# Optimization experiments

Measured on AMD Instinct MI355X. Metric: run time of the kernel, lower is better.

## Reference

```python
import jax, jax.numpy as jnp
import numpy as np

N_HEADS = 16
HEAD_DIM = 64


def apply_rope(x, cos, sin):
    # x: [B, H, S, D]; cos/sin: [S, D//2]
    x_even = x[..., ::2]
    x_odd = x[..., 1::2]
    c = cos[None, None, :, :]
    s = sin[None, None, :, :]
    rot_even = x_even * c - x_odd * s
    rot_odd = x_even * s + x_odd * c
    return jnp.stack((rot_even, rot_odd), axis=-1).reshape(x.shape)


def setup_inputs() -> dict:
    key = jax.random.key(0)
    ks = jax.random.split(key, 7)
    B, S, D = 2, 2048, 1024
    x = jax.random.normal(ks[0], (B, S, D), dtype=jnp.float32)
    # realistic rope tables
    inv_freq = 1.0 / (10000.0 ** (np.arange(0, HEAD_DIM, 2, dtype=np.float32) / HEAD_DIM))
    t = np.arange(S, dtype=np.float32)
    freqs = np.outer(t, inv_freq)  # [S, HEAD_DIM//2]
    rope_cos = jnp.asarray(np.cos(freqs), dtype=jnp.float32)
    rope_sin = jnp.asarray(np.sin(freqs), dtype=jnp.float32)
    Wqkv = jax.random.normal(ks[1], (D, 3 * D), dtype=jnp.float32) * (D ** -0.5)
    bqkv = jax.random.normal(ks[2], (3 * D,), dtype=jnp.float32) * 0.02
    Wout = jax.random.normal(ks[3], (D, D), dtype=jnp.float32) * (D ** -0.5)
    bout = jax.random.normal(ks[4], (D,), dtype=jnp.float32) * 0.02
    return {"x": x, "rope_cos": rope_cos, "rope_sin": rope_sin,
            "Wqkv": Wqkv, "bqkv": bqkv, "Wout": Wout, "bout": bout}


def reference(x, rope_cos, rope_sin, Wqkv, bqkv, Wout, bout):
    B, S, D = x.shape
    H, Hd = N_HEADS, HEAD_DIM
    qkv = x @ Wqkv + bqkv                      # [B, S, 3D]
    qkv = qkv.reshape(B, S, 3, H, Hd).transpose(2, 0, 3, 1, 4)  # [3, B, H, S, Hd]
    q, k, v = qkv[0], qkv[1], qkv[2]
    q = apply_rope(q, rope_cos, rope_sin)
    k = apply_rope(k, rope_cos, rope_sin)
    scale = Hd ** -0.5
    scores = jnp.einsum('bhqd,bhkd->bhqk', q, k) * scale
    causal = jnp.tril(jnp.ones((S, S), dtype=bool))
    scores = jnp.where(causal[None, None], scores, jnp.finfo(scores.dtype).min)
    attn = jax.nn.softmax(scores, axis=-1)
    out = jnp.einsum('bhqk,bhkd->bhqd', attn, v)  # [B, H, S, Hd]
    out = out.transpose(0, 2, 1, 3).reshape(B, S, D)
    return out @ Wout + bout
```

## Files before the change

### kernel.cpp

```cpp
#include <hip/hip_runtime.h>
#include <hip/hip_bf16.h>

typedef unsigned short u16;
typedef __attribute__((ext_vector_type(4))) float f32x4;
typedef __attribute__((ext_vector_type(16))) float f32x16;
typedef __attribute__((ext_vector_type(8))) short short8;
typedef __attribute__((ext_vector_type(8))) unsigned short ushort8;

#define AS1 __attribute__((address_space(1)))
#define AS3 __attribute__((address_space(3)))

__device__ __forceinline__ u16 f2bf(float f) {
  union { float f; unsigned u; } v; v.f = f;
  unsigned r = v.u + 0x7fffu + ((v.u >> 16) & 1u);
  return (u16)(r >> 16);
}
__device__ __forceinline__ float b2f(u16 h) {
  union { unsigned u; float f; } v; v.u = ((unsigned)h) << 16;
  return v.f;
}
__device__ __forceinline__ f32x4 mfma16(short8 a, short8 b, f32x4 c) {
  return __builtin_amdgcn_mfma_f32_16x16x32_bf16(a, b, c, 0, 0, 0);
}
__device__ __forceinline__ f32x16 mfma32(short8 a, short8 b, f32x16 c) {
  return __builtin_amdgcn_mfma_f32_32x32x16_bf16(a, b, c, 0, 0, 0);
}
__device__ __forceinline__ unsigned cvtpk(float a, float b) {
  unsigned r;
  asm("v_cvt_pk_bf16_f32 %0, %1, %2" : "=v"(r) : "v"(a), "v"(b));
  return r;
}
__device__ __forceinline__ short8 pack4(unsigned w0, unsigned w1, unsigned w2, unsigned w3) {
  union { unsigned u[4]; short8 s; } t;
  t.u[0] = w0; t.u[1] = w1; t.u[2] = w2; t.u[3] = w3;
  return t.s;
}
__device__ __forceinline__ float exp2h(float x) { return __builtin_amdgcn_exp2f(x); }

__global__ __launch_bounds__(256) void cvt_f32_bf16_k(const float* __restrict__ in,
                                                      u16* __restrict__ out, int n8) {
  int t = blockIdx.x * 256 + threadIdx.x;
  if (t >= n8) return;
  const float4* p = (const float4*)(in + (size_t)t * 8);
  float4 a = p[0], b = p[1];
  ushort8 o;
  o[0] = f2bf(a.x); o[1] = f2bf(a.y); o[2] = f2bf(a.z); o[3] = f2bf(a.w);
  o[4] = f2bf(b.x); o[5] = f2bf(b.y); o[6] = f2bf(b.z); o[7] = f2bf(b.w);
  *(ushort8*)(out + (size_t)t * 8) = o;
}

__global__ __launch_bounds__(256) void transpose_f32_bf16_k(const float* __restrict__ in,
                                                            u16* __restrict__ out, int R, int C) {
  __shared__ float tile[32][33];
  int bc = blockIdx.x * 32, br = blockIdx.y * 32;
  int tx = threadIdx.x & 31, ty = threadIdx.x >> 5;
#pragma unroll
  for (int p = 0; p < 4; ++p)
    tile[ty + p * 8][tx] = in[(size_t)(br + ty + p * 8) * C + bc + tx];
  __syncthreads();
#pragma unroll
  for (int p = 0; p < 4; ++p)
    out[(size_t)(bc + ty + p * 8) * R + br + tx] = f2bf(tile[tx][ty + p * 8]);
}

template <int MODE>
__global__ __launch_bounds__(256) void gemm_bt_k(const u16* __restrict__ A,
                                                 const u16* __restrict__ Bt,
                                                 const float* __restrict__ bias,
                                                 const float* __restrict__ cosT,
                                                 const float* __restrict__ sinT,
                                                 void* __restrict__ Cout) {
  __shared__ __align__(16) u16 As[128 * 32];
  __shared__ __align__(16) u16 Bs[128 * 32];
  const int tid = threadIdx.x, lane = tid & 63, w = tid >> 6;
  const int wr = w >> 1, wc = w & 1, g = lane >> 4, c16 = lane & 15;
  const int rowBase = blockIdx.y * 128, colBase = blockIdx.x * 128;
  f32x4 acc[4][4] = {};
  const int e0 = (w * 2 + 0) * 512 + lane * 8;
  const int e1 = (w * 2 + 1) * 512 + lane * 8;
  const u16* Ag0 = A + (size_t)(rowBase + (e0 >> 5)) * 1024 + (e0 & 31);
  const u16* Ag1 = A + (size_t)(rowBase + (e1 >> 5)) * 1024 + (e1 & 31);
  const u16* Bg0 = Bt + (size_t)(colBase + (e0 >> 5)) * 1024 + (e0 & 31);
  const u16* Bg1 = Bt + (size_t)(colBase + (e1 >> 5)) * 1024 + (e1 & 31);
  u16* As0 = As + (w * 2 + 0) * 512;
  u16* As1 = As + (w * 2 + 1) * 512;
  u16* Bs0 = Bs + (w * 2 + 0) * 512;
  u16* Bs1 = Bs + (w * 2 + 1) * 512;
  for (int k0 = 0; k0 < 1024; k0 += 32) {
    __builtin_amdgcn_global_load_lds((const AS1 void*)(Ag0 + k0), (AS3 void*)As0, 16, 0, 0);
    __builtin_amdgcn_global_load_lds((const AS1 void*)(Ag1 + k0), (AS3 void*)As1, 16, 0, 0);
    __builtin_amdgcn_global_load_lds((const AS1 void*)(Bg0 + k0), (AS3 void*)Bs0, 16, 0, 0);
    __builtin_amdgcn_global_load_lds((const AS1 void*)(Bg1 + k0), (AS3 void*)Bs1, 16, 0, 0);
    asm volatile("s_waitcnt vmcnt(0)" ::: "memory");
    __syncthreads();
    short8 af[4], bfr[4];
#pragma unroll
    for (int t = 0; t < 4; ++t)
      af[t] = *(const short8*)(As + ((wr * 64 + t * 16 + c16) * 32 + g * 8));
#pragma unroll
    for (int t = 0; t < 4; ++t)
      bfr[t] = *(const short8*)(Bs + ((wc * 64 + t * 16 + c16) * 32 + g * 8));
#pragma unroll
    for (int i = 0; i < 4; ++i)
#pragma unroll
      for (int j = 0; j < 4; ++j) acc[i][j] = mfma16(af[i], bfr[j], acc[i][j]);
    __syncthreads();
  }
#pragma unroll
  for (int i = 0; i < 4; ++i) {
    int mbase = rowBase + wr * 64 + i * 16 + 4 * g;
#pragma unroll
    for (int j = 0; j < 4; ++j) {
      int n = colBase + wc * 64 + j * 16 + c16;
      float bv = bias[n];
#pragma unroll
      for (int r = 0; r < 4; ++r) {
        float v = acc[i][j][r] + bv;
        int m = mbase + r;
        if (MODE == 0) {
          int which = n >> 10, hh = (n >> 6) & 15, d = n & 63;
          int bb = m >> 11, s = m & 2047;
          float outv = v;
          if (which < 2) {
            float pv = __shfl_xor(v, 1);
            float cc = cosT[(size_t)s * 32 + (d >> 1)];
            float ss = sinT[(size_t)s * 32 + (d >> 1)];
            outv = (d & 1) ? (v * cc + pv * ss) : (v * cc - pv * ss);
            if (which == 0) outv *= 0.18033688f;
          }
          ((u16*)Cout)[((size_t)(((which * 2 + bb) * 16 + hh) * 2048 + s) << 6) + d] = f2bf(outv);
        } else {
          ((float*)Cout)[(size_t)m * 1024 + n] = v;
        }
      }
    }
  }
}

__global__ __launch_bounds__(256) void vtrans_k(const u16* __restrict__ V, u16* __restrict__ Vt) {
  __shared__ u16 t[64][72];
  const int bh = blockIdx.y, s0 = blockIdx.x * 64;
  const u16* src = V + ((size_t)bh << 17);
  u16* dst = Vt + ((size_t)bh << 17);
  const int r = threadIdx.x >> 2, c0 = (threadIdx.x & 3) * 16;
  *(short8*)&t[r][c0] = *(const short8*)(src + (size_t)(s0 + r) * 64 + c0);
  *(short8*)&t[r][c0 + 8] = *(const short8*)(src + (size_t)(s0 + r) * 64 + c0 + 8);
  __syncthreads();
  const int d = threadIdx.x >> 2, sc0 = (threadIdx.x & 3) * 16;
  ushort8 o0, o1;
#pragma unroll
  for (int e = 0; e < 8; ++e) { o0[e] = t[sc0 + e][d]; o1[e] = t[sc0 + 8 + e][d]; }
  *(ushort8*)(dst + (size_t)d * 2048 + s0 + sc0) = o0;
  *(ushort8*)(dst + (size_t)d * 2048 + s0 + sc0 + 8) = o1;
}

__global__ __launch_bounds__(128, 4) void attn8_k(const u16* __restrict__ Qm,
                                                  const u16* __restrict__ Km,
                                                  const u16* __restrict__ Vtm,
                                                  u16* __restrict__ Om) {
  __shared__ __align__(16) u16 KL[2][4096];
  __shared__ __align__(16) u16 VL[2][4096];

  const int tid = threadIdx.x;
  const int lane = tid & 63, w = tid >> 6;
  const int x = blockIdx.x & 7;
  const int i = blockIdx.x >> 3;
  const int bh = 4 * x + (i & 3);
  const int rank = i >> 2;
  const int sl = rank >> 3, g8 = rank & 7;
  const int qm = (sl & 1) ? (8 * sl + 7 - g8) : (8 * sl + g8);
  const int b = bh >> 4, hd = bh & 15;
  const int qb = qm * 64 + w * 32;
  const int q32 = lane & 31, hl = lane >> 5;
  const int nt = qm + 1;

  const u16* Qp = Qm + ((size_t)bh << 17);
  const u16* Kp = Km + ((size_t)bh << 17);
  const u16* Vtp = Vtm + ((size_t)bh << 17);

  const u16* qrow = Qp + ((size_t)(qb + q32) << 6) + 8 * hl;
  short8 qf[4];
#pragma unroll
  for (int ks = 0; ks < 4; ++ks) qf[ks] = *(const short8*)(qrow + 16 * ks);

  f32x16 acc0 = {}, acc1 = {};
  float m_run = -1e30f, l_run = 0.f;
  const int qg = qb + q32;
  const int r8 = lane >> 3;
  const int sb = (lane & 7) ^ r8;
  const int swz = q32 & 7;

  auto stage = [&](int buf, int k0s) {
#pragma unroll
    for (int j = 0; j < 4; ++j) {
      const int row = j * 16 + w * 8 + r8;
      const u16* ksrc = Kp + ((size_t)(k0s + row) << 6) + sb * 8;
      __builtin_amdgcn_global_load_lds(
          (const AS1 void*)ksrc,
          (AS3 void*)(&KL[buf][(j * 16 + w * 8) * 64]), 16, 0, 0);
      const u16* vsrc = Vtp + ((size_t)row << 11) + k0s + sb * 8;
      __builtin_amdgcn_global_load_lds(
          (const AS1 void*)vsrc,
          (AS3 void*)(&VL[buf][(j * 16 + w * 8) * 64]), 16, 0, 0);
    }
  };

  stage(0, 0);
  asm volatile("s_waitcnt vmcnt(0)" ::: "memory");
  __syncthreads();

  for (int it = 0; it < nt; ++it) {
    const int cur = it & 1;
    if (it + 1 < nt) stage(cur ^ 1, 64 * (it + 1));
    const int k0 = 64 * it;

    const u16* Kb = &KL[cur][0];
    const u16* Vb = &VL[cur][0];

    f32x16 s0 = {}, s1 = {};
    __builtin_amdgcn_s_setprio(1);
#pragma unroll
    for (int ks = 0; ks < 4; ++ks) {
      const int cb = ((2 * ks + hl) ^ swz) * 8;
      short8 kf0 = *(const short8*)(Kb + q32 * 64 + cb);
      short8 kf1 = *(const short8*)(Kb + (32 + q32) * 64 + cb);
      s0 = mfma32(kf0, qf[ks], s0);
      s1 = mfma32(kf1, qf[ks], s1);
    }
    __builtin_amdgcn_s_setprio(0);

    short8 vfa[4], vfb[4];
#pragma unroll
    for (int ks = 0; ks < 4; ++ks) {
      const int cb = ((2 * ks + hl) ^ swz) * 8;
      vfa[ks] = *(const short8*)(Vb + q32 * 64 + cb);
      vfb[ks] = *(const short8*)(Vb + (32 + q32) * 64 + cb);
    }

    if (k0 + 63 > qb) {
#pragma unroll
      for (int r = 0; r < 16; ++r) {
        const int kvl = k0 + (r & 3) + 8 * (r >> 2) + 4 * hl;
        s0[r] = (kvl <= qg) ? s0[r] : -1e30f;
        s1[r] = (kvl + 32 <= qg) ? s1[r] : -1e30f;
      }
    }

    float pmax = s0[0];
#pragma unroll
    for (int r = 1; r < 16; ++r) pmax = fmaxf(pmax, s0[r]);
#pragma unroll
    for (int r = 0; r < 16; ++r) pmax = fmaxf(pmax, s1[r]);
    pmax = fmaxf(pmax, __shfl_xor(pmax, 32));

    if (!__all(pmax <= m_run + 11.5f)) {
      const float mn = fmaxf(m_run, pmax);
      const float alpha = exp2h(m_run - mn);
      l_run *= alpha;
      m_run = mn;
#pragma unroll
      for (int r = 0; r < 16; ++r) {
        const int row = (r & 3) + 8 * (r >> 2) + 4 * hl;
        const float ar = __shfl(alpha, row);
        acc0[r] *= ar; acc1[r] *= ar;
      }
    }

    float rs = 0.f;
#pragma unroll
    for (int r = 0; r < 16; ++r) { s0[r] = exp2h(s0[r] - m_run); rs += s0[r]; }
#pragma unroll
    for (int r = 0; r < 16; ++r) { s1[r] = exp2h(s1[r] - m_run); rs += s1[r]; }
    rs += __shfl_xor(rs, 32);
    l_run += rs;

    short8 pa[4];
#pragma unroll
    for (int t = 0; t < 2; ++t) {
      float p0, p1, p2, p3, p4, p5, p6, p7, p8, p9, pa_, pb_, pc_, pd_, pe_, pf_;
      if (t == 0) {
        p0 = s0[0];  p1 = s0[1];  p2 = s0[2];  p3 = s0[3];
        p4 = s0[4];  p5 = s0[5];  p6 = s0[6];  p7 = s0[7];
        p8 = s0[8];  p9 = s0[9];  pa_ = s0[10]; pb_ = s0[11];
        pc_ = s0[12]; pd_ = s0[13]; pe_ = s0[14]; pf_ = s0[15];
      } else {
        p0 = s1[0];  p1 = s1[1];  p2 = s1[2];  p3 = s1[3];
        p4 = s1[4];  p5 = s1[5];  p6 = s1[6];  p7 = s1[7];
        p8 = s1[8];  p9 = s1[9];  pa_ = s1[10]; pb_ = s1[11];
        pc_ = s1[12]; pd_ = s1[13]; pe_ = s1[14]; pf_ = s1[15];
      }
      const unsigned a0 = cvtpk(p0, p1), a1 = cvtpk(p2, p3);
      const unsigned a2 = cvtpk(p4, p5), a3 = cvtpk(p6, p7);
      const unsigned b0 = cvtpk(p8, p9), b1 = cvtpk(pa_, pb_);
      const unsigned b2 = cvtpk(pc_, pd_), b3 = cvtpk(pe_, pf_);
      const unsigned r0 = __shfl_xor(hl ? a0 : a2, 32);
      const unsigned r1 = __shfl_xor(hl ? a1 : a3, 32);
      pa[2 * t] = hl ? pack4(r0, r1, a2, a3) : pack4(a0, a1, r0, r1);
      const unsigned r2 = __shfl_xor(hl ? b0 : b2, 32);
      const unsigned r3 = __shfl_xor(hl ? b1 : b3, 32);
      pa[2 * t + 1] = hl ? pack4(r2, r3, b2, b3) : pack4(b0, b1, r2, r3);
    }

    __builtin_amdgcn_s_setprio(1);
#pragma unroll
    for (int ks = 0; ks < 4; ++ks) {
      acc0 = mfma32(pa[ks], vfa[ks], acc0);
      acc1 = mfma32(pa[ks], vfb[ks], acc1);
    }
    __builtin_amdgcn_s_setprio(0);

    asm volatile("s_waitcnt vmcnt(0)" ::: "memory");
    __syncthreads();
  }

#pragma unroll
  for (int r = 0; r < 16; ++r) {
    const int row = (r & 3) + 8 * (r >> 2) + 4 * hl;
    const float li = 1.0f / __shfl(l_run, row);
    const int q = qb + row;
    const size_t base = ((size_t)(b * 2048 + q) << 10) + hd * 64 + q32;
    Om[base] = f2bf(acc0[r] * li);
    Om[base + 32] = f2bf(acc1[r] * li);
  }
}

extern "C" void kernel_launch(void* const* d_in, const int* in_sizes, int n_in,
                              void* d_out, int out_size, void* d_ws, size_t ws_size,
                              hipStream_t stream) {
  const float* x        = (const float*)d_in[0];
  const float* rope_cos = (const float*)d_in[1];
  const float* rope_sin = (const float*)d_in[2];
  const float* Wqkv     = (const float*)d_in[3];
  const float* bqkv     = (const float*)d_in[4];
  const float* Wout     = (const float*)d_in[5];
  const float* bout     = (const float*)d_in[6];
  float* out = (float*)d_out;
  char* ws = (char*)d_ws;

  u16* Xb      = (u16*)(ws);
  u16* WqkvT   = (u16*)(ws + 8388608);
  u16* WoutT   = (u16*)(ws + 14680064);
  u16* QKV     = (u16*)(ws + 16777216);
  u16* AttnOut = (u16*)(ws + 41943040);
  u16* Vt      = (u16*)(ws + 50331648);

  cvt_f32_bf16_k<<<dim3(2048), dim3(256), 0, stream>>>(x, Xb, 524288);
  transpose_f32_bf16_k<<<dim3(96, 32), dim3(256), 0, stream>>>(Wqkv, WqkvT, 1024, 3072);
  transpose_f32_bf16_k<<<dim3(32, 32), dim3(256), 0, stream>>>(Wout, WoutT, 1024, 1024);

  gemm_bt_k<0><<<dim3(24, 32), dim3(256), 0, stream>>>(Xb, WqkvT, bqkv, rope_cos, rope_sin,
                                                       (void*)QKV);

  u16* Qw = QKV;
  u16* Kw = QKV + (size_t)4194304;
  u16* Vw = QKV + (size_t)8388608;
  vtrans_k<<<dim3(32, 32), dim3(256), 0, stream>>>(Vw, Vt);
  attn8_k<<<dim3(1024), dim3(128), 0, stream>>>(Qw, Kw, Vt, AttnOut);

  gemm_bt_k<1><<<dim3(8, 32), dim3(256), 0, stream>>>(AttnOut, WoutT, bout, nullptr, nullptr, out);
}
```

Measured before the change: 145.0 us.

## Enlarge attention tiles to 128 queries and 128 keys per block with four waves

The attention kernel now uses 256-thread blocks that each own 128 query rows, and it processes 128-key tiles per iteration with double-buffered K and V in LDS. The V tile gets a new swizzle. V fragments are loaded just in time inside each PV sub-step, and sub-tiles lying entirely above the diagonal are skipped on the last tile. The aim is to halve the grid and the number of loop iterations, sharing each staged K/V tile across more query rows to cut global traffic and sync overhead. In exchange it uses more LDS and registers per block, lowers occupancy, and increases load imbalance from the causal structure, since the block order changes from 1024 to 512 blocks.

```diff
diff --git a/kernel.cpp b/kernel.cpp
--- a/kernel.cpp
+++ b/kernel.cpp
@@ -154,12 +154,12 @@
   *(ushort8*)(dst + (size_t)d * 2048 + s0 + sc0 + 8) = o1;
 }
 
-__global__ __launch_bounds__(128, 4) void attn8_k(const u16* __restrict__ Qm,
+__global__ __launch_bounds__(256, 2) void attn9_k(const u16* __restrict__ Qm,
                                                   const u16* __restrict__ Km,
                                                   const u16* __restrict__ Vtm,
                                                   u16* __restrict__ Om) {
-  __shared__ __align__(16) u16 KL[2][4096];
-  __shared__ __align__(16) u16 VL[2][4096];
+  __shared__ __align__(16) u16 KL[2][8192];
+  __shared__ __align__(16) u16 VL[2][8192];
 
   const int tid = threadIdx.x;
   const int lane = tid & 63, w = tid >> 6;
@@ -167,10 +167,9 @@
   const int i = blockIdx.x >> 3;
   const int bh = 4 * x + (i & 3);
   const int rank = i >> 2;
-  const int sl = rank >> 3, g8 = rank & 7;
-  const int qm = (sl & 1) ? (8 * sl + 7 - g8) : (8 * sl + g8);
+  const int qm = (rank < 8) ? (15 - rank) : (rank - 8);
   const int b = bh >> 4, hd = bh & 15;
-  const int qb = qm * 64 + w * 32;
+  const int qb = qm * 128 + w * 32;
   const int q32 = lane & 31, hl = lane >> 5;
   const int nt = qm + 1;
 
@@ -185,23 +184,25 @@
 
   f32x16 acc0 = {}, acc1 = {};
   float m_run = -1e30f, l_run = 0.f;
-  const int qg = qb + q32;
-  const int r8 = lane >> 3;
-  const int sb = (lane & 7) ^ r8;
   const int swz = q32 & 7;
+  const int swz4 = q32 & 15;
+  const int kr = lane >> 3;
+  const int kcb = (lane & 7) ^ kr;
+  const int vr = lane >> 4;
 
   auto stage = [&](int buf, int k0s) {
 #pragma unroll
     for (int j = 0; j < 4; ++j) {
-      const int row = j * 16 + w * 8 + r8;
-      const u16* ksrc = Kp + ((size_t)(k0s + row) << 6) + sb * 8;
+      const int ck = w * 4 + j;
+      const int krow = ck * 8 + kr;
       __builtin_amdgcn_global_load_lds(
-          (const AS1 void*)ksrc,
-          (AS3 void*)(&KL[buf][(j * 16 + w * 8) * 64]), 16, 0, 0);
-      const u16* vsrc = Vtp + ((size_t)row << 11) + k0s + sb * 8;
+          (const AS1 void*)(Kp + ((size_t)(k0s + krow) << 6) + kcb * 8),
+          (AS3 void*)(&KL[buf][ck * 512]), 16, 0, 0);
+      const int vrow = ck * 4 + vr;
+      const int vcb = (lane & 15) ^ (vrow & 15);
       __builtin_amdgcn_global_load_lds(
-          (const AS1 void*)vsrc,
-          (AS3 void*)(&VL[buf][(j * 16 + w * 8) * 64]), 16, 0, 0);
+          (const AS1 void*)(Vtp + ((size_t)vrow << 11) + k0s + vcb * 8),
+          (AS3 void*)(&VL[buf][ck * 512]), 16, 0, 0);
     }
   };
 
@@ -209,40 +210,35 @@
   asm volatile("s_waitcnt vmcnt(0)" ::: "memory");
   __syncthreads();
 
-  for (int it = 0; it < nt; ++it) {
-    const int cur = it & 1;
-    if (it + 1 < nt) stage(cur ^ 1, 64 * (it + 1));
-    const int k0 = 64 * it;
+  for (int kt = 0; kt < nt; ++kt) {
+    const int cur = kt & 1;
+    if (kt + 1 < nt) stage(cur ^ 1, 128 * (kt + 1));
+    const bool last = (kt == nt - 1);
 
     const u16* Kb = &KL[cur][0];
     const u16* Vb = &VL[cur][0];
 
-    f32x16 s0 = {}, s1 = {};
+    f32x16 s0 = {}, s1 = {}, s2 = {}, s3 = {};
     __builtin_amdgcn_s_setprio(1);
 #pragma unroll
     for (int ks = 0; ks < 4; ++ks) {
       const int cb = ((2 * ks + hl) ^ swz) * 8;
-      short8 kf0 = *(const short8*)(Kb + q32 * 64 + cb);
-      short8 kf1 = *(const short8*)(Kb + (32 + q32) * 64 + cb);
-      s0 = mfma32(kf0, qf[ks], s0);
-      s1 = mfma32(kf1, qf[ks], s1);
+      s0 = mfma32(*(const short8*)(Kb + (q32) * 64 + cb), qf[ks], s0);
+      s1 = mfma32(*(const short8*)(Kb + (32 + q32) * 64 + cb), qf[ks], s1);
+      s2 = mfma32(*(const short8*)(Kb + (64 + q32) * 64 + cb), qf[ks], s2);
+      s3 = mfma32(*(const short8*)(Kb + (96 + q32) * 64 + cb), qf[ks], s3);
     }
     __builtin_amdgcn_s_setprio(0);
 
-    short8 vfa[4], vfb[4];
-#pragma unroll
-    for (int ks = 0; ks < 4; ++ks) {
-      const int cb = ((2 * ks + hl) ^ swz) * 8;
-      vfa[ks] = *(const short8*)(Vb + q32 * 64 + cb);
-      vfb[ks] = *(const short8*)(Vb + (32 + q32) * 64 + cb);
-    }
-
-    if (k0 + 63 > qb) {
+    if (last) {
+      const int qloc = 32 * w + q32;
 #pragma unroll
       for (int r = 0; r < 16; ++r) {
-        const int kvl = k0 + (r & 3) + 8 * (r >> 2) + 4 * hl;
-        s0[r] = (kvl <= qg) ? s0[r] : -1e30f;
-        s1[r] = (kvl + 32 <= qg) ? s1[r] : -1e30f;
+        const int crow = (r & 3) + 8 * (r >> 2) + 4 * hl;
+        s0[r] = (crow <= qloc) ? s0[r] : -1e30f;
+        s1[r] = (32 + crow <= qloc) ? s1[r] : -1e30f;
+        s2[r] = (64 + crow <= qloc) ? s2[r] : -1e30f;
+        s3[r] = (96 + crow <= qloc) ? s3[r] : -1e30f;
       }
     }
 
@@ -251,6 +247,10 @@
     for (int r = 1; r < 16; ++r) pmax = fmaxf(pmax, s0[r]);
 #pragma unroll
     for (int r = 0; r < 16; ++r) pmax = fmaxf(pmax, s1[r]);
+#pragma unroll
+    for (int r = 0; r < 16; ++r) pmax = fmaxf(pmax, s2[r]);
+#pragma unroll
+    for (int r = 0; r < 16; ++r) pmax = fmaxf(pmax, s3[r]);
     pmax = fmaxf(pmax, __shfl_xor(pmax, 32));
 
     if (!__all(pmax <= m_run + 11.5f)) {
@@ -271,43 +271,44 @@
     for (int r = 0; r < 16; ++r) { s0[r] = exp2h(s0[r] - m_run); rs += s0[r]; }
 #pragma unroll
     for (int r = 0; r < 16; ++r) { s1[r] = exp2h(s1[r] - m_run); rs += s1[r]; }
+#pragma unroll
+    for (int r = 0; r < 16; ++r) { s2[r] = exp2h(s2[r] - m_run); rs += s2[r]; }
+#pragma unroll
+    for (int r = 0; r < 16; ++r) { s3[r] = exp2h(s3[r] - m_run); rs += s3[r]; }
     rs += __shfl_xor(rs, 32);
     l_run += rs;
 
-    short8 pa[4];
-#pragma unroll
-    for (int t = 0; t < 2; ++t) {
-      float p0, p1, p2, p3, p4, p5, p6, p7, p8, p9, pa_, pb_, pc_, pd_, pe_, pf_;
-      if (t == 0) {
-        p0 = s0[0];  p1 = s0[1];  p2 = s0[2];  p3 = s0[3];
-        p4 = s0[4];  p5 = s0[5];  p6 = s0[6];  p7 = s0[7];
-        p8 = s0[8];  p9 = s0[9];  pa_ = s0[10]; pb_ = s0[11];
-        pc_ = s0[12]; pd_ = s0[13]; pe_ = s0[14]; pf_ = s0[15];
-      } else {
-        p0 = s1[0];  p1 = s1[1];  p2 = s1[2];  p3 = s1[3];
-        p4 = s1[4];  p5 = s1[5];  p6 = s1[6];  p7 = s1[7];
-        p8 = s1[8];  p9 = s1[9];  pa_ = s1[10]; pb_ = s1[11];
-        pc_ = s1[12]; pd_ = s1[13]; pe_ = s1[14]; pf_ = s1[15];
-      }
-      const unsigned a0 = cvtpk(p0, p1), a1 = cvtpk(p2, p3);
-      const unsigned a2 = cvtpk(p4, p5), a3 = cvtpk(p6, p7);
-      const unsigned b0 = cvtpk(p8, p9), b1 = cvtpk(pa_, pb_);
-      const unsigned b2 = cvtpk(pc_, pd_), b3 = cvtpk(pe_, pf_);
-      const unsigned r0 = __shfl_xor(hl ? a0 : a2, 32);
-      const unsigned r1 = __shfl_xor(hl ? a1 : a3, 32);
-      pa[2 * t] = hl ? pack4(r0, r1, a2, a3) : pack4(a0, a1, r0, r1);
-      const unsigned r2 = __shfl_xor(hl ? b0 : b2, 32);
-      const unsigned r3 = __shfl_xor(hl ? b1 : b3, 32);
-      pa[2 * t + 1] = hl ? pack4(r2, r3, b2, b3) : pack4(b0, b1, r2, r3);
-    }
-
-    __builtin_amdgcn_s_setprio(1);
-#pragma unroll
-    for (int ks = 0; ks < 4; ++ks) {
-      acc0 = mfma32(pa[ks], vfa[ks], acc0);
-      acc1 = mfma32(pa[ks], vfb[ks], acc1);
-    }
-    __builtin_amdgcn_s_setprio(0);
+    auto pvsub = [&](const f32x16& sv, int t) {
+      short8 p0, p1;
+      {
+        const unsigned a0 = cvtpk(sv[0], sv[1]), a1 = cvtpk(sv[2], sv[3]);
+        const unsigned a2 = cvtpk(sv[4], sv[5]), a3 = cvtpk(sv[6], sv[7]);
+        const unsigned b0 = cvtpk(sv[8], sv[9]), b1 = cvtpk(sv[10], sv[11]);
+        const unsigned b2 = cvtpk(sv[12], sv[13]), b3 = cvtpk(sv[14], sv[15]);
+        const unsigned r0 = __shfl_xor(hl ? a0 : a2, 32);
+        const unsigned r1 = __shfl_xor(hl ? a1 : a3, 32);
+        p0 = hl ? pack4(r0, r1, a2, a3) : pack4(a0, a1, r0, r1);
+        const unsigned r2 = __shfl_xor(hl ? b0 : b2, 32);
+        const unsigned r3 = __shfl_xor(hl ? b1 : b3, 32);
+        p1 = hl ? pack4(r2, r3, b2, b3) : pack4(b0, b1, r2, r3);
+      }
+      __builtin_amdgcn_s_setprio(1);
+#pragma unroll
+      for (int j = 0; j < 2; ++j) {
+        const short8 pj = j ? p1 : p0;
+        const int cbv = ((4 * t + 2 * j + hl) ^ swz4) * 8;
+        const short8 vf0 = *(const short8*)(Vb + q32 * 128 + cbv);
+        const short8 vf1 = *(const short8*)(Vb + (32 + q32) * 128 + cbv);
+        acc0 = mfma32(pj, vf0, acc0);
+        acc1 = mfma32(pj, vf1, acc1);
+      }
+      __builtin_amdgcn_s_setprio(0);
+    };
+
+    pvsub(s0, 0);
+    if (!last || w >= 1) pvsub(s1, 1);
+    if (!last || w >= 2) pvsub(s2, 2);
+    if (!last || w >= 3) pvsub(s3, 3);
 
     asm volatile("s_waitcnt vmcnt(0)" ::: "memory");
     __syncthreads();
@@ -355,7 +356,7 @@
   u16* Kw = QKV + (size_t)4194304;
   u16* Vw = QKV + (size_t)8388608;
   vtrans_k<<<dim3(32, 32), dim3(256), 0, stream>>>(Vw, Vt);
-  attn8_k<<<dim3(1024), dim3(128), 0, stream>>>(Qw, Kw, Vt, AttnOut);
+  attn9_k<<<dim3(512), dim3(256), 0, stream>>>(Qw, Kw, Vt, AttnOut);
 
   gemm_bt_k<1><<<dim3(8, 32), dim3(256), 0, stream>>>(AttnOut, WoutT, bout, nullptr, nullptr, out);
 }
```

New measurement: 133.8 us. 1.08x faster.

## Use 128-row query blocks with split-KV for long rows plus merge kernel

Applied to the files above, without the earlier changes.

The attention kernel now uses 4 waves per block covering 128 query rows, so each staged K/V tile is shared by twice as many queries. For the upper 8 query blocks the KV range is split in two halves handled by separate blocks, each writing unnormalized bf16 partial accumulators and running max/sum to workspace. A new merge kernel combines the two halves. This is meant to cut K/V reload traffic and balance causal work across blocks, at the cost of an extra launch, partial-result traffic, bf16 rounding of the partials, and reuse of the Xb workspace region.

```diff
diff --git a/kernel.cpp b/kernel.cpp
--- a/kernel.cpp
+++ b/kernel.cpp
@@ -154,25 +154,28 @@
   *(ushort8*)(dst + (size_t)d * 2048 + s0 + sc0 + 8) = o1;
 }
 
-__global__ __launch_bounds__(128, 4) void attn8_k(const u16* __restrict__ Qm,
-                                                  const u16* __restrict__ Km,
-                                                  const u16* __restrict__ Vtm,
-                                                  u16* __restrict__ Om) {
+__global__ __launch_bounds__(256, 3) void attn10_k(const u16* __restrict__ Qm,
+                                                   const u16* __restrict__ Km,
+                                                   const u16* __restrict__ Vtm,
+                                                   u16* __restrict__ Pacc,
+                                                   float* __restrict__ Ml,
+                                                   u16* __restrict__ Om) {
   __shared__ __align__(16) u16 KL[2][4096];
   __shared__ __align__(16) u16 VL[2][4096];
 
   const int tid = threadIdx.x;
   const int lane = tid & 63, w = tid >> 6;
   const int x = blockIdx.x & 7;
-  const int i = blockIdx.x >> 3;
-  const int bh = 4 * x + (i & 3);
-  const int rank = i >> 2;
-  const int sl = rank >> 3, g8 = rank & 7;
-  const int qm = (sl & 1) ? (8 * sl + 7 - g8) : (8 * sl + g8);
+  const int idx = blockIdx.x >> 3;
+  const int j = idx & 3, u = idx >> 2;
+  const int bh = 4 * x + j;
+  int qm, t0, t1, half;
+  bool split;
+  if (u < 8) { qm = u; split = false; half = 0; t0 = 0; t1 = 2 * u + 2; }
+  else { split = true; half = (u >= 16); qm = 15 - (u & 7); t0 = half ? (qm + 1) : 0; t1 = t0 + qm + 1; }
   const int b = bh >> 4, hd = bh & 15;
-  const int qb = qm * 64 + w * 32;
+  const int qb = qm * 128 + w * 32;
   const int q32 = lane & 31, hl = lane >> 5;
-  const int nt = qm + 1;
 
   const u16* Qp = Qm + ((size_t)bh << 17);
   const u16* Kp = Km + ((size_t)bh << 17);
@@ -186,141 +189,193 @@
   f32x16 acc0 = {}, acc1 = {};
   float m_run = -1e30f, l_run = 0.f;
   const int qg = qb + q32;
-  const int r8 = lane >> 3;
-  const int sb = (lane & 7) ^ r8;
+  const int rr = w * 8 + (lane >> 3);
+  const int sb = (lane & 7) ^ (lane >> 3);
   const int swz = q32 & 7;
 
   auto stage = [&](int buf, int k0s) {
-#pragma unroll
-    for (int j = 0; j < 4; ++j) {
-      const int row = j * 16 + w * 8 + r8;
-      const u16* ksrc = Kp + ((size_t)(k0s + row) << 6) + sb * 8;
-      __builtin_amdgcn_global_load_lds(
-          (const AS1 void*)ksrc,
-          (AS3 void*)(&KL[buf][(j * 16 + w * 8) * 64]), 16, 0, 0);
-      const u16* vsrc = Vtp + ((size_t)row << 11) + k0s + sb * 8;
-      __builtin_amdgcn_global_load_lds(
-          (const AS1 void*)vsrc,
-          (AS3 void*)(&VL[buf][(j * 16 + w * 8) * 64]), 16, 0, 0);
-    }
+    u16* kb = &KL[buf][w * 512];
+    u16* vb = &VL[buf][w * 512];
+    __builtin_amdgcn_global_load_lds(
+        (const AS1 void*)(Kp + ((size_t)(k0s + rr) << 6) + sb * 8),
+        (AS3 void*)kb, 16, 0, 0);
+    __builtin_amdgcn_global_load_lds(
+        (const AS1 void*)(Kp + ((size_t)(k0s + rr + 32) << 6) + sb * 8),
+        (AS3 void*)(kb + 2048), 16, 0, 0);
+    __builtin_amdgcn_global_load_lds(
+        (const AS1 void*)(Vtp + ((size_t)rr << 11) + k0s + sb * 8),
+        (AS3 void*)vb, 16, 0, 0);
+    __builtin_amdgcn_global_load_lds(
+        (const AS1 void*)(Vtp + ((size_t)(rr + 32) << 11) + k0s + sb * 8),
+        (AS3 void*)(vb + 2048), 16, 0, 0);
   };
 
-  stage(0, 0);
+  stage(0, 64 * t0);
   asm volatile("s_waitcnt vmcnt(0)" ::: "memory");
   __syncthreads();
 
-  for (int it = 0; it < nt; ++it) {
-    const int cur = it & 1;
-    if (it + 1 < nt) stage(cur ^ 1, 64 * (it + 1));
+  for (int it = t0; it < t1; ++it) {
+    const int cur = (it - t0) & 1;
+    if (it + 1 < t1) stage(cur ^ 1, 64 * (it + 1));
     const int k0 = 64 * it;
 
-    const u16* Kb = &KL[cur][0];
-    const u16* Vb = &VL[cur][0];
-
-    f32x16 s0 = {}, s1 = {};
-    __builtin_amdgcn_s_setprio(1);
-#pragma unroll
-    for (int ks = 0; ks < 4; ++ks) {
-      const int cb = ((2 * ks + hl) ^ swz) * 8;
-      short8 kf0 = *(const short8*)(Kb + q32 * 64 + cb);
-      short8 kf1 = *(const short8*)(Kb + (32 + q32) * 64 + cb);
-      s0 = mfma32(kf0, qf[ks], s0);
-      s1 = mfma32(kf1, qf[ks], s1);
+    if (k0 <= qb + 31) {
+      const u16* Kb = &KL[cur][0];
+      const u16* Vb = &VL[cur][0];
+
+      f32x16 s0 = {}, s1 = {};
+      __builtin_amdgcn_s_setprio(1);
+#pragma unroll
+      for (int ks = 0; ks < 4; ++ks) {
+        const int cb = ((2 * ks + hl) ^ swz) * 8;
+        short8 kf0 = *(const short8*)(Kb + q32 * 64 + cb);
+        short8 kf1 = *(const short8*)(Kb + (32 + q32) * 64 + cb);
+        s0 = mfma32(kf0, qf[ks], s0);
+        s1 = mfma32(kf1, qf[ks], s1);
+      }
+      __builtin_amdgcn_s_setprio(0);
+
+      short8 vfa[4], vfb[4];
+#pragma unroll
+      for (int ks = 0; ks < 4; ++ks) {
+        const int cb = ((2 * ks + hl) ^ swz) * 8;
+        vfa[ks] = *(const short8*)(Vb + q32 * 64 + cb);
+        vfb[ks] = *(const short8*)(Vb + (32 + q32) * 64 + cb);
+      }
+
+      if (k0 + 63 > qb) {
+#pragma unroll
+        for (int r = 0; r < 16; ++r) {
+          const int kvl = k0 + (r & 3) + 8 * (r >> 2) + 4 * hl;
+          s0[r] = (kvl <= qg) ? s0[r] : -1e30f;
+          s1[r] = (kvl + 32 <= qg) ? s1[r] : -1e30f;
+        }
+      }
+
+      float pmax = s0[0];
+#pragma unroll
+      for (int r = 1; r < 16; ++r) pmax = fmaxf(pmax, s0[r]);
+#pragma unroll
+      for (int r = 0; r < 16; ++r) pmax = fmaxf(pmax, s1[r]);
+      pmax = fmaxf(pmax, __shfl_xor(pmax, 32));
+
+      if (!__all(pmax <= m_run + 11.5f)) {
+        const float mn = fmaxf(m_run, pmax);
+        const float alpha = exp2h(m_run - mn);
+        l_run *= alpha;
+        m_run = mn;
+#pragma unroll
+        for (int r = 0; r < 16; ++r) {
+          const int row = (r & 3) + 8 * (r >> 2) + 4 * hl;
+          const float ar = __shfl(alpha, row);
+          acc0[r] *= ar; acc1[r] *= ar;
+        }
+      }
+
+      float rs = 0.f;
+#pragma unroll
+      for (int r = 0; r < 16; ++r) { s0[r] = exp2h(s0[r] - m_run); rs += s0[r]; }
+#pragma unroll
+      for (int r = 0; r < 16; ++r) { s1[r] = exp2h(s1[r] - m_run); rs += s1[r]; }
+      rs += __shfl_xor(rs, 32);
+      l_run += rs;
+
+      short8 pa[4];
+#pragma unroll
+      for (int t = 0; t < 2; ++t) {
+        float p0, p1, p2, p3, p4, p5, p6, p7, p8, p9, pa_, pb_, pc_, pd_, pe_, pf_;
+        if (t == 0) {
+          p0 = s0[0];  p1 = s0[1];  p2 = s0[2];  p3 = s0[3];
+          p4 = s0[4];  p5 = s0[5];  p6 = s0[6];  p7 = s0[7];
+          p8 = s0[8];  p9 = s0[9];  pa_ = s0[10]; pb_ = s0[11];
+          pc_ = s0[12]; pd_ = s0[13]; pe_ = s0[14]; pf_ = s0[15];
+        } else {
+          p0 = s1[0];  p1 = s1[1];  p2 = s1[2];  p3 = s1[3];
+          p4 = s1[4];  p5 = s1[5];  p6 = s1[6];  p7 = s1[7];
+          p8 = s1[8];  p9 = s1[9];  pa_ = s1[10]; pb_ = s1[11];
+          pc_ = s1[12]; pd_ = s1[13]; pe_ = s1[14]; pf_ = s1[15];
+        }
+        const unsigned a0 = cvtpk(p0, p1), a1 = cvtpk(p2, p3);
+        const unsigned a2 = cvtpk(p4, p5), a3 = cvtpk(p6, p7);
+        const unsigned b0 = cvtpk(p8, p9), b1 = cvtpk(pa_, pb_);
+        const unsigned b2 = cvtpk(pc_, pd_), b3 = cvtpk(pe_, pf_);
+        const unsigned r0 = __shfl_xor(hl ? a0 : a2, 32);
+        const unsigned r1 = __shfl_xor(hl ? a1 : a3, 32);
+        pa[2 * t] = hl ? pack4(r0, r1, a2, a3) : pack4(a0, a1, r0, r1);
+        const unsigned r2 = __shfl_xor(hl ? b0 : b2, 32);
+        const unsigned r3 = __shfl_xor(hl ? b1 : b3, 32);
+        pa[2 * t + 1] = hl ? pack4(r2, r3, b2, b3) : pack4(b0, b1, r2, r3);
+      }
+
+      __builtin_amdgcn_s_setprio(1);
+#pragma unroll
+      for (int ks = 0; ks < 4; ++ks) {
+        acc0 = mfma32(pa[ks], vfa[ks], acc0);
+        acc1 = mfma32(pa[ks], vfb[ks], acc1);
+      }
+      __builtin_amdgcn_s_setprio(0);
     }
-    __builtin_amdgcn_s_setprio(0);
-
-    short8 vfa[4], vfb[4];
-#pragma unroll
-    for (int ks = 0; ks < 4; ++ks) {
-      const int cb = ((2 * ks + hl) ^ swz) * 8;
-      vfa[ks] = *(const short8*)(Vb + q32 * 64 + cb);
-      vfb[ks] = *(const short8*)(Vb + (32 + q32) * 64 + cb);
-    }
-
-    if (k0 + 63 > qb) {
-#pragma unroll
-      for (int r = 0; r < 16; ++r) {
-        const int kvl = k0 + (r & 3) + 8 * (r >> 2) + 4 * hl;
-        s0[r] = (kvl <= qg) ? s0[r] : -1e30f;
-        s1[r] = (kvl + 32 <= qg) ? s1[r] : -1e30f;
-      }
-    }
-
-    float pmax = s0[0];
-#pragma unroll
-    for (int r = 1; r < 16; ++r) pmax = fmaxf(pmax, s0[r]);
-#pragma unroll
-    for (int r = 0; r < 16; ++r) pmax = fmaxf(pmax, s1[r]);
-    pmax = fmaxf(pmax, __shfl_xor(pmax, 32));
-
-    if (!__all(pmax <= m_run + 11.5f)) {
-      const float mn = fmaxf(m_run, pmax);
-      const float alpha = exp2h(m_run - mn);
-      l_run *= alpha;
-      m_run = mn;
-#pragma unroll
-      for (int r = 0; r < 16; ++r) {
-        const int row = (r & 3) + 8 * (r >> 2) + 4 * hl;
-        const float ar = __shfl(alpha, row);
-        acc0[r] *= ar; acc1[r] *= ar;
-      }
-    }
-
-    float rs = 0.f;
-#pragma unroll
-    for (int r = 0; r < 16; ++r) { s0[r] = exp2h(s0[r] - m_run); rs += s0[r]; }
-#pragma unroll
-    for (int r = 0; r < 16; ++r) { s1[r] = exp2h(s1[r] - m_run); rs += s1[r]; }
-    rs += __shfl_xor(rs, 32);
-    l_run += rs;
-
-    short8 pa[4];
-#pragma unroll
-    for (int t = 0; t < 2; ++t) {
-      float p0, p1, p2, p3, p4, p5, p6, p7, p8, p9, pa_, pb_, pc_, pd_, pe_, pf_;
-      if (t == 0) {
-        p0 = s0[0];  p1 = s0[1];  p2 = s0[2];  p3 = s0[3];
-        p4 = s0[4];  p5 = s0[5];  p6 = s0[6];  p7 = s0[7];
-        p8 = s0[8];  p9 = s0[9];  pa_ = s0[10]; pb_ = s0[11];
-        pc_ = s0[12]; pd_ = s0[13]; pe_ = s0[14]; pf_ = s0[15];
-      } else {
-        p0 = s1[0];  p1 = s1[1];  p2 = s1[2];  p3 = s1[3];
-        p4 = s1[4];  p5 = s1[5];  p6 = s1[6];  p7 = s1[7];
-        p8 = s1[8];  p9 = s1[9];  pa_ = s1[10]; pb_ = s1[11];
-        pc_ = s1[12]; pd_ = s1[13]; pe_ = s1[14]; pf_ = s1[15];
-      }
-      const unsigned a0 = cvtpk(p0, p1), a1 = cvtpk(p2, p3);
-      const unsigned a2 = cvtpk(p4, p5), a3 = cvtpk(p6, p7);
-      const unsigned b0 = cvtpk(p8, p9), b1 = cvtpk(pa_, pb_);
-      const unsigned b2 = cvtpk(pc_, pd_), b3 = cvtpk(pe_, pf_);
-      const unsigned r0 = __shfl_xor(hl ? a0 : a2, 32);
-      const unsigned r1 = __shfl_xor(hl ? a1 : a3, 32);
-      pa[2 * t] = hl ? pack4(r0, r1, a2, a3) : pack4(a0, a1, r0, r1);
-      const unsigned r2 = __shfl_xor(hl ? b0 : b2, 32);
-      const unsigned r3 = __shfl_xor(hl ? b1 : b3, 32);
-      pa[2 * t + 1] = hl ? pack4(r2, r3, b2, b3) : pack4(b0, b1, r2, r3);
-    }
-
-    __builtin_amdgcn_s_setprio(1);
-#pragma unroll
-    for (int ks = 0; ks < 4; ++ks) {
-      acc0 = mfma32(pa[ks], vfa[ks], acc0);
-      acc1 = mfma32(pa[ks], vfb[ks], acc1);
-    }
-    __builtin_amdgcn_s_setprio(0);
 
     asm volatile("s_waitcnt vmcnt(0)" ::: "memory");
     __syncthreads();
   }
 
-#pragma unroll
-  for (int r = 0; r < 16; ++r) {
-    const int row = (r & 3) + 8 * (r >> 2) + 4 * hl;
-    const float li = 1.0f / __shfl(l_run, row);
-    const int q = qb + row;
-    const size_t base = ((size_t)(b * 2048 + q) << 10) + hd * 64 + q32;
-    Om[base] = f2bf(acc0[r] * li);
-    Om[base + 32] = f2bf(acc1[r] * li);
+  if (!split) {
+#pragma unroll
+    for (int r = 0; r < 16; ++r) {
+      const int row = (r & 3) + 8 * (r >> 2) + 4 * hl;
+      const float li = 1.0f / __shfl(l_run, row);
+      const int q = qb + row;
+      const size_t base = ((size_t)(b * 2048 + q) << 10) + hd * 64 + q32;
+      Om[base] = f2bf(acc0[r] * li);
+      Om[base + 32] = f2bf(acc1[r] * li);
+    }
+  } else {
+    const int slot = half * 256 + bh * 8 + (qm - 8);
+    u16* pacc = Pacc + (size_t)slot * 8192;
+#pragma unroll
+    for (int r = 0; r < 16; ++r) {
+      const int row = (r & 3) + 8 * (r >> 2) + 4 * hl;
+      const int rl = w * 32 + row;
+      pacc[rl * 64 + q32] = f2bf(acc0[r]);
+      pacc[rl * 64 + q32 + 32] = f2bf(acc1[r]);
+    }
+    if (hl == 0) {
+      Ml[(size_t)slot * 128 + w * 32 + q32] = m_run;
+      Ml[65536 + (size_t)slot * 128 + w * 32 + q32] = l_run;
+    }
+  }
+}
+
+__global__ __launch_bounds__(256) void merge10_k(const u16* __restrict__ Pacc,
+                                                 const float* __restrict__ Ml,
+                                                 u16* __restrict__ Om) {
+  const int x = blockIdx.x & 7;
+  const int t = blockIdx.x >> 3;
+  const int j = t & 3, qs = t >> 2;
+  const int bh = 4 * x + j, qm = 8 + qs;
+  const int b = bh >> 4, hd = bh & 15;
+  const int s0 = bh * 8 + qs, s1 = 256 + s0;
+  const u16* a0p = Pacc + (size_t)s0 * 8192;
+  const u16* a1p = Pacc + (size_t)s1 * 8192;
+#pragma unroll
+  for (int k = 0; k < 4; ++k) {
+    const int i = threadIdx.x + 256 * k;
+    const int row = i >> 3, co = (i & 7) * 8;
+    const float m0 = Ml[(size_t)s0 * 128 + row];
+    const float m1 = Ml[(size_t)s1 * 128 + row];
+    const float l0 = Ml[65536 + (size_t)s0 * 128 + row];
+    const float l1 = Ml[65536 + (size_t)s1 * 128 + row];
+    const float M = fmaxf(m0, m1);
+    const float e0 = exp2h(m0 - M), e1 = exp2h(m1 - M);
+    const float li = 1.0f / (l0 * e0 + l1 * e1);
+    const ushort8 A0 = *(const ushort8*)(a0p + row * 64 + co);
+    const ushort8 A1 = *(const ushort8*)(a1p + row * 64 + co);
+    ushort8 o;
+#pragma unroll
+    for (int e = 0; e < 8; ++e)
+      o[e] = f2bf((b2f(A0[e]) * e0 + b2f(A1[e]) * e1) * li);
+    *(ushort8*)(Om + ((size_t)(b * 2048 + qm * 128 + row) << 10) + hd * 64 + co) = o;
   }
 }
 
@@ -344,6 +399,9 @@
   u16* AttnOut = (u16*)(ws + 41943040);
   u16* Vt      = (u16*)(ws + 50331648);
 
+  u16* Pacc = (u16*)(ws);
+  float* Ml = (float*)(ws + 8388608);
+
   cvt_f32_bf16_k<<<dim3(2048), dim3(256), 0, stream>>>(x, Xb, 524288);
   transpose_f32_bf16_k<<<dim3(96, 32), dim3(256), 0, stream>>>(Wqkv, WqkvT, 1024, 3072);
   transpose_f32_bf16_k<<<dim3(32, 32), dim3(256), 0, stream>>>(Wout, WoutT, 1024, 1024);
@@ -355,7 +413,9 @@
   u16* Kw = QKV + (size_t)4194304;
   u16* Vw = QKV + (size_t)8388608;
   vtrans_k<<<dim3(32, 32), dim3(256), 0, stream>>>(Vw, Vt);
-  attn8_k<<<dim3(1024), dim3(128), 0, stream>>>(Qw, Kw, Vt, AttnOut);
+
+  attn10_k<<<dim3(768), dim3(256), 0, stream>>>(Qw, Kw, Vt, Pacc, Ml, AttnOut);
+  merge10_k<<<dim3(256), dim3(256), 0, stream>>>(Pacc, Ml, AttnOut);
 
   gemm_bt_k<1><<<dim3(8, 32), dim3(256), 0, stream>>>(AttnOut, WoutT, bout, nullptr, nullptr, out);
 }
```

New measurement: 128.6 us (median of 3 runs). 11.3% less time.
